# Kernel tuning notes

Hardware: AMD Instinct MI355X
Metric: run time of the kernel (lower is better)

The kernel has to match this reference:

```python
import jax, jax.numpy as jnp
import numpy as np

EPS = 1.55e-5  # tf.math.l2_normalize epsilon semantics: x / sqrt(max(sum(x^2), eps))


def _l2norm_tokens(t):
    # normalize over the token axis (-2), matching tf.math.l2_normalize(axis=-2)
    sq = jnp.sum(t * t, axis=-2, keepdims=True)
    return t * jax.lax.rsqrt(jnp.maximum(sq, EPS))


def setup_inputs() -> dict:
    key = jax.random.key(0)
    ks = jax.random.split(key, 4)
    B, H, W, C = 16, 64, 64, 512
    heads = 8
    return {
        "x": jax.random.normal(ks[0], (B, H, W, C), jnp.float32),
        "qkv_w": jax.random.normal(ks[1], (C, 3 * C), jnp.float32) * (C ** -0.5),
        "q_bias": jnp.zeros((C,), jnp.float32),
        "v_bias": jnp.zeros((C,), jnp.float32),
        "scale": jnp.ones((heads, 1, 1), jnp.float32),
        "proj_w": jax.random.normal(ks[2], (C, C), jnp.float32) * (C ** -0.5),
        "proj_b": jnp.zeros((C,), jnp.float32),
    }


def reference(x, qkv_w, q_bias, v_bias, scale, proj_w, proj_b):
    B, H, W, C = x.shape
    heads = scale.shape[0]
    d = C // heads
    N = H * W

    # 1x1 conv QKV (no conv bias) + concatenated [q_bias, 0, v_bias]
    qkv = jnp.einsum("bhwc,cf->bhwf", x, qkv_w)
    qkv = qkv + jnp.concatenate([q_bias, jnp.zeros_like(q_bias), v_bias])
    # [B, N, heads, 3, d] -> [B, heads, N, 3, d]
    qkv = qkv.reshape(B, N, heads, 3, d).transpose(0, 2, 1, 3, 4)
    q, k, v = qkv[..., 0, :], qkv[..., 1, :], qkv[..., 2, :]  # each [B, heads, N, d]

    q = _l2norm_tokens(q)
    k = _l2norm_tokens(k)

    # channel-attention: [B, heads, d, d]
    attn = jnp.einsum("bhnd,bhne->bhde", q * jnp.exp(scale), k)
    attn = jax.nn.softmax(attn, axis=-1)

    # matmul(attn, v^T) -> [B, heads, d, N]; perm [0,3,1,2] -> [B, N, heads, d]
    out = jnp.einsum("bhde,bhne->bhdn", attn, v)
    out = out.transpose(0, 3, 1, 2).reshape(B, H, W, C)

    # output 1x1 conv projection with bias
    return jnp.einsum("bhwc,cf->bhwf", out, proj_w) + proj_b
```

## Files before the change

### kernel.cpp

```cpp
#include <hip/hip_runtime.h>
#include <stdint.h>
#include <stddef.h>

#define BATCH  16
#define HEADS  8
#define NTOK   4096
#define CDIM   512
#define FDIM   1536

typedef short bf16x8 __attribute__((ext_vector_type(8)));
typedef float fx4    __attribute__((ext_vector_type(4)));

__device__ __forceinline__ uint16_t f2bf(float f) {
    uint32_t u = __float_as_uint(f);
    return (uint16_t)((u + 0x7FFFu + ((u >> 16) & 1u)) >> 16);
}
__device__ __forceinline__ float bf2f(uint16_t u) {
    return __uint_as_float(((uint32_t)u) << 16);
}
__device__ __forceinline__ void gload16(const uint16_t* g, uint16_t* l) {
    __builtin_amdgcn_global_load_lds(
        (const __attribute__((address_space(1))) uint32_t*)(g),
        (__attribute__((address_space(3))) uint32_t*)(l), 16, 0, 0);
}
__device__ __forceinline__ int cidx(int row, int col) {
    return row * 128 + (col ^ ((row & 7) << 3));
}

__global__ void transpose_w_kernel(const float* __restrict__ qkv_w,
                                   const float* __restrict__ proj_w,
                                   uint16_t* __restrict__ Wt,
                                   uint16_t* __restrict__ Pt) {
    __shared__ uint16_t tile[32][33];
    int blk = blockIdx.x;
    const float* src; uint16_t* dst; int W, Hh, r0, c0;
    if (blk < 768) {
        int tr = blk / 48, tc = blk % 48;
        src = qkv_w; dst = Wt; W = 1536; Hh = 512; r0 = tr * 32; c0 = tc * 32;
    } else {
        blk -= 768;
        int tr = blk / 16, tc = blk % 16;
        src = proj_w; dst = Pt; W = 512; Hh = 512; r0 = tr * 32; c0 = tc * 32;
    }
    const int tx = threadIdx.x & 31, ty = threadIdx.x >> 5;
    #pragma unroll
    for (int j = 0; j < 4; j++)
        tile[ty + 8 * j][tx] = f2bf(src[(size_t)(r0 + ty + 8 * j) * W + c0 + tx]);
    __syncthreads();
    #pragma unroll
    for (int j = 0; j < 4; j++)
        dst[(size_t)(c0 + ty + 8 * j) * Hh + r0 + tx] = tile[tx][ty + 8 * j];
}

__global__ void prep_kernel(const float* __restrict__ X,
                            uint16_t* __restrict__ Xb,
                            float* __restrict__ Sqk) {
    const int tid = blockIdx.x * blockDim.x + threadIdx.x;
    const int stride = gridDim.x * blockDim.x;
    for (int i = tid; i < (1 << 22); i += stride) {
        const fx4* src = reinterpret_cast<const fx4*>(X + (size_t)i * 8);
        fx4 v0 = src[0], v1 = src[1];
        union { bf16x8 v; uint16_t u[8]; } pk;
        #pragma unroll
        for (int e = 0; e < 4; e++) { pk.u[e] = f2bf(v0[e]); pk.u[4 + e] = f2bf(v1[e]); }
        reinterpret_cast<bf16x8*>(Xb)[i] = pk.v;
    }
    for (int i = tid; i < 16384; i += stride) Sqk[i] = 0.0f;
}

__global__ __launch_bounds__(256) void gemm_qkv_kernel(
        const uint16_t* __restrict__ Xb, const uint16_t* __restrict__ Wt,
        const float* __restrict__ q_bias, const float* __restrict__ v_bias,
        uint16_t* __restrict__ QT, uint16_t* __restrict__ KT,
        uint16_t* __restrict__ VT,
        float* __restrict__ Sq, float* __restrict__ Sk) {
    __shared__ uint16_t sh[128 * 128];
    uint16_t* As = sh;
    uint16_t* Bs = sh + 8192;
    const int bx = blockIdx.x;
    const int swz = (bx & 7) * 768 + (bx >> 3);
    const int tm = swz / 12, tn = swz % 12;
    const int gm = tm * 128, gn = tn * 128;
    const int b = gm >> 12, tok0 = gm & 4095;
    const int t = threadIdx.x, lane = t & 63, w = t >> 6;
    const int wm = w >> 1, wn = w & 1;
    const int l15 = lane & 15, lg = lane >> 4;
    fx4 acc[4][4] = {};
    const int skey = (t >> 3) & 7;
    const int scol0 = ((t & 7) ^ skey) * 8;
    for (int k0 = 0; k0 < 512; k0 += 64) {
        const uint16_t* ga = Xb + (size_t)(gm + (t >> 3)) * 512 + k0 + scol0;
        const uint16_t* gb = Wt + (size_t)(gn + (t >> 3)) * 512 + k0 + scol0;
        uint16_t* la = &As[t * 8];
        uint16_t* lb = &Bs[t * 8];
        #pragma unroll
        for (int j = 0; j < 4; j++) {
            gload16(ga + (size_t)j * 32 * 512, la + j * 2048);
            gload16(gb + (size_t)j * 32 * 512, lb + j * 2048);
        }
        __syncthreads();
        #pragma unroll
        for (int ks = 0; ks < 2; ks++) {
            const int kof = ks * 32 + lg * 8;
            bf16x8 af[4], bfr[4];
            #pragma unroll
            for (int m = 0; m < 4; m++) {
                const int row = wm * 64 + m * 16 + l15;
                af[m] = *reinterpret_cast<const bf16x8*>(&As[row * 64 + (kof ^ ((row & 7) << 3))]);
            }
            #pragma unroll
            for (int n = 0; n < 4; n++) {
                const int row = wn * 64 + n * 16 + l15;
                bfr[n] = *reinterpret_cast<const bf16x8*>(&Bs[row * 64 + (kof ^ ((row & 7) << 3))]);
            }
            #pragma unroll
            for (int m = 0; m < 4; m++)
                #pragma unroll
                for (int n = 0; n < 4; n++)
                    acc[m][n] = __builtin_amdgcn_mfma_f32_16x16x32_bf16(
                        af[m], bfr[n], acc[m][n], 0, 0, 0);
        }
        __syncthreads();
    }
    #pragma unroll
    for (int n = 0; n < 4; n++) {
        const int col = gn + wn * 64 + n * 16 + l15;
        const float bias = (col < 512) ? q_bias[col]
                          : ((col < 1024) ? 0.0f : v_bias[col - 1024]);
        #pragma unroll
        for (int m = 0; m < 4; m++)
            #pragma unroll
            for (int r = 0; r < 4; r++) {
                const int lrow = wm * 64 + m * 16 + lg * 4 + r;
                const int lcol = wn * 64 + n * 16 + l15;
                sh[cidx(lrow, lcol)] = f2bf(acc[m][n][r] + bias);
            }
    }
    __syncthreads();
    const int cc = t >> 7, tloc = t & 127;
    const int u = (gn >> 6) + cc;
    const int h = u / 3, which = u % 3;
    const int bh = b * 8 + h;
    if (which < 2) {
        const int d = tloc & 63, oct = tloc >> 6;
        uint16_t* dst = (which == 0 ? QT : KT)
                        + ((size_t)bh * 64 + d) * 4096 + tok0 + oct * 64;
        float ss = 0.f;
        #pragma unroll
        for (int g = 0; g < 8; g++) {
            union { bf16x8 v; uint16_t u16v[8]; } pk;
            #pragma unroll
            for (int s2 = 0; s2 < 8; s2++) {
                uint16_t val = sh[cidx(oct * 64 + g * 8 + s2, cc * 64 + d)];
                pk.u16v[s2] = val;
                float f = bf2f(val);
                ss += f * f;
            }
            *reinterpret_cast<bf16x8*>(dst + g * 8) = pk.v;
        }
        atomicAdd((which == 0 ? Sq : Sk) + bh * 64 + d, ss);
    } else {
        const int tok = tloc;
        uint16_t* dst = VT + (size_t)(gm + tok) * 512 + h * 64;
        #pragma unroll
        for (int bb = 0; bb < 8; bb++) {
            bf16x8 v = *reinterpret_cast<const bf16x8*>(&sh[cidx(tok, cc * 64 + bb * 8)]);
            *reinterpret_cast<bf16x8*>(dst + bb * 8) = v;
        }
    }
}

__global__ __launch_bounds__(256) void attn_qk_kernel(
        const uint16_t* __restrict__ QT, const uint16_t* __restrict__ KT,
        float* __restrict__ Gpart) {
    __shared__ uint16_t Qs[64 * 128];
    __shared__ uint16_t Ks[64 * 128];
    const int blk = blockIdx.x;
    const int bh = blk >> 2, quarter = blk & 3;
    const int t = threadIdx.x, lane = t & 63, w = t >> 6;
    const int l15 = lane & 15, lg = lane >> 4;
    const int wr = w >> 1, wc = w & 1;
    fx4 acc[2][2] = {};
    const uint16_t* qbase = QT + (size_t)bh * 64 * 4096;
    const uint16_t* kbase = KT + (size_t)bh * 64 * 4096;
    for (int it = 0; it < 8; it++) {
        const int tokt = quarter * 1024 + it * 128;
        #pragma unroll
        for (int j = 0; j < 4; j++) {
            const int li = j * 256 + t;
            const int row = li >> 4;
            const int src_off = (((li & 15) ^ (row & 7)) << 3);
            gload16(qbase + (size_t)row * 4096 + tokt + src_off, &Qs[li * 8]);
            gload16(kbase + (size_t)row * 4096 + tokt + src_off, &Ks[li * 8]);
        }
        __syncthreads();
        #pragma unroll
        for (int ks = 0; ks < 4; ks++) {
            const int kof = ks * 32 + lg * 8;
            const int ra0 = wr * 32 + l15,      ra1 = wr * 32 + 16 + l15;
            const int rb0 = wc * 32 + l15,      rb1 = wc * 32 + 16 + l15;
            bf16x8 a0 = *reinterpret_cast<const bf16x8*>(&Qs[ra0 * 128 + (kof ^ ((ra0 & 7) << 3))]);
            bf16x8 a1 = *reinterpret_cast<const bf16x8*>(&Qs[ra1 * 128 + (kof ^ ((ra1 & 7) << 3))]);
            bf16x8 b0 = *reinterpret_cast<const bf16x8*>(&Ks[rb0 * 128 + (kof ^ ((rb0 & 7) << 3))]);
            bf16x8 b1 = *reinterpret_cast<const bf16x8*>(&Ks[rb1 * 128 + (kof ^ ((rb1 & 7) << 3))]);
            acc[0][0] = __builtin_amdgcn_mfma_f32_16x16x32_bf16(a0, b0, acc[0][0], 0, 0, 0);
            acc[0][1] = __builtin_amdgcn_mfma_f32_16x16x32_bf16(a0, b1, acc[0][1], 0, 0, 0);
            acc[1][0] = __builtin_amdgcn_mfma_f32_16x16x32_bf16(a1, b0, acc[1][0], 0, 0, 0);
            acc[1][1] = __builtin_amdgcn_mfma_f32_16x16x32_bf16(a1, b1, acc[1][1], 0, 0, 0);
        }
        __syncthreads();
    }
    float* gp = Gpart + (size_t)quarter * 524288 + (size_t)bh * 4096;
    #pragma unroll
    for (int mi = 0; mi < 2; mi++)
        #pragma unroll
        for (int ni = 0; ni < 2; ni++)
            #pragma unroll
            for (int r = 0; r < 4; r++) {
                const int d = wr * 32 + mi * 16 + lg * 4 + r;
                const int e = wc * 32 + ni * 16 + l15;
                gp[d * 64 + e] = acc[mi][ni][r];
            }
}

__global__ void attn_finalize_kernel(const float* __restrict__ Gpart,
                                     const float* __restrict__ Sq,
                                     const float* __restrict__ Sk,
                                     const float* __restrict__ scale,
                                     uint16_t* __restrict__ attnb) {
    const int bh = blockIdx.x;
    const int h = bh & 7;
    const int t = threadIdx.x;
    const int e = t & 63, w = t >> 6;
    const float es = expf(scale[h]);
    const float rk = rsqrtf(fmaxf(Sk[bh * 64 + e], 1.55e-5f));
    const float* g0 = Gpart + (size_t)bh * 4096;
    for (int d = w; d < 64; d += 4) {
        const float rq = rsqrtf(fmaxf(Sq[bh * 64 + d], 1.55e-5f));
        float g = g0[d * 64 + e] + g0[524288 + d * 64 + e]
                + g0[1048576 + d * 64 + e] + g0[1572864 + d * 64 + e];
        float x = es * g * rq * rk;
        float m = x;
        #pragma unroll
        for (int off = 32; off; off >>= 1) m = fmaxf(m, __shfl_xor(m, off, 64));
        float p = expf(x - m);
        float s = p;
        #pragma unroll
        for (int off = 32; off; off >>= 1) s += __shfl_xor(s, off, 64);
        attnb[(size_t)bh * 4096 + d * 64 + e] = f2bf(p / s);
    }
}

__global__ __launch_bounds__(256) void pv_kernel(
        const uint16_t* __restrict__ VT, const uint16_t* __restrict__ attnb,
        uint16_t* __restrict__ out_t) {
    __shared__ uint16_t Vs[64 * 64];
    const int blk = blockIdx.x;
    const int bh = blk >> 6, chunk = blk & 63;
    const int b = bh >> 3, h = bh & 7;
    const int n0 = chunk * 64;
    const int t = threadIdx.x, lane = t & 63, w = t >> 6;
    const int l15 = lane & 15, lg = lane >> 4;
    #pragma unroll
    for (int j = 0; j < 2; j++) {
        const int li = j * 256 + t;
        const int row = li >> 3;
        const int src_off = (((li & 7) ^ (row & 7)) << 3);
        gload16(VT + (size_t)(b * NTOK + n0 + row) * 512 + h * 64 + src_off, &Vs[li * 8]);
    }
    bf16x8 bfr[4][2];
    const uint16_t* ab = attnb + (size_t)bh * 4096;
    #pragma unroll
    for (int n = 0; n < 4; n++)
        #pragma unroll
        for (int ks = 0; ks < 2; ks++)
            bfr[n][ks] = *reinterpret_cast<const bf16x8*>(ab + (n * 16 + l15) * 64 + ks * 32 + lg * 8);
    __syncthreads();
    fx4 acc[4] = {};
    #pragma unroll
    for (int ks = 0; ks < 2; ks++) {
        const int row = w * 16 + l15;
        const int kof = ks * 32 + lg * 8;
        bf16x8 a = *reinterpret_cast<const bf16x8*>(&Vs[row * 64 + (kof ^ ((row & 7) << 3))]);
        #pragma unroll
        for (int n = 0; n < 4; n++)
            acc[n] = __builtin_amdgcn_mfma_f32_16x16x32_bf16(a, bfr[n][ks], acc[n], 0, 0, 0);
    }
    #pragma unroll
    for (int n = 0; n < 4; n++)
        #pragma unroll
        for (int r = 0; r < 4; r++) {
            const int tokg = b * NTOK + n0 + w * 16 + lg * 4 + r;
            out_t[(size_t)tokg * CDIM + h * 64 + n * 16 + l15] = f2bf(acc[n][r]);
        }
}

__global__ __launch_bounds__(256) void gemm_proj_kernel(
        const uint16_t* __restrict__ At, const uint16_t* __restrict__ Pt,
        const float* __restrict__ proj_b, float* __restrict__ outp) {
    __shared__ uint16_t As[128 * 64];
    __shared__ uint16_t Bs[128 * 64];
    const int bx = blockIdx.x;
    const int swz = (bx & 7) * 256 + (bx >> 3);
    const int tn = swz & 3, tm = swz >> 2;
    const int gm = tm * 128, gn = tn * 128;
    const int t = threadIdx.x, lane = t & 63, w = t >> 6;
    const int wm = w >> 1, wn = w & 1;
    const int l15 = lane & 15, lg = lane >> 4;
    fx4 acc[4][4] = {};
    const int skey = (t >> 3) & 7;
    const int scol0 = ((t & 7) ^ skey) * 8;
    for (int k0 = 0; k0 < 512; k0 += 64) {
        const uint16_t* ga = At + (size_t)(gm + (t >> 3)) * 512 + k0 + scol0;
        const uint16_t* gb = Pt + (size_t)(gn + (t >> 3)) * 512 + k0 + scol0;
        #pragma unroll
        for (int j = 0; j < 4; j++) {
            gload16(ga + (size_t)j * 32 * 512, &As[t * 8 + j * 2048]);
            gload16(gb + (size_t)j * 32 * 512, &Bs[t * 8 + j * 2048]);
        }
        __syncthreads();
        #pragma unroll
        for (int ks = 0; ks < 2; ks++) {
            const int kof = ks * 32 + lg * 8;
            bf16x8 af[4], bfr[4];
            #pragma unroll
            for (int m = 0; m < 4; m++) {
                const int row = wm * 64 + m * 16 + l15;
                af[m] = *reinterpret_cast<const bf16x8*>(&As[row * 64 + (kof ^ ((row & 7) << 3))]);
            }
            #pragma unroll
            for (int n = 0; n < 4; n++) {
                const int row = wn * 64 + n * 16 + l15;
                bfr[n] = *reinterpret_cast<const bf16x8*>(&Bs[row * 64 + (kof ^ ((row & 7) << 3))]);
            }
            #pragma unroll
            for (int m = 0; m < 4; m++)
                #pragma unroll
                for (int n = 0; n < 4; n++)
                    acc[m][n] = __builtin_amdgcn_mfma_f32_16x16x32_bf16(
                        af[m], bfr[n], acc[m][n], 0, 0, 0);
        }
        __syncthreads();
    }
    #pragma unroll
    for (int m = 0; m < 4; m++) {
        #pragma unroll
        for (int n = 0; n < 4; n++) {
            const int col = gn + wn * 64 + n * 16 + l15;
            const float bias = proj_b[col];
            #pragma unroll
            for (int r = 0; r < 4; r++) {
                const int row = gm + wm * 64 + m * 16 + lg * 4 + r;
                outp[(size_t)row * CDIM + col] = acc[m][n][r] + bias;
            }
        }
    }
}

extern "C" void kernel_launch(void* const* d_in, const int* in_sizes, int n_in,
                              void* d_out, int out_size, void* d_ws, size_t ws_size,
                              hipStream_t stream) {
    (void)in_sizes; (void)n_in; (void)out_size; (void)ws_size;
    const float* x      = (const float*)d_in[0];
    const float* qkv_w  = (const float*)d_in[1];
    const float* q_bias = (const float*)d_in[2];
    const float* v_bias = (const float*)d_in[3];
    const float* scale  = (const float*)d_in[4];
    const float* proj_w = (const float*)d_in[5];
    const float* proj_b = (const float*)d_in[6];
    float* out = (float*)d_out;

    char* wsp = (char*)d_ws;
    uint16_t* Wt    = (uint16_t*)(wsp);
    uint16_t* Pt    = (uint16_t*)(wsp + 1572864);
    float*    Sq    = (float*)   (wsp + 2097152);
    float*    Sk    = (float*)   (wsp + 2129920);
    float*    Gpart = (float*)   (wsp + 2162688);
    uint16_t* attnb = (uint16_t*)(wsp + 10551296);
    uint16_t* QT    = (uint16_t*)(wsp + 11599872);
    uint16_t* KT    = (uint16_t*)(wsp + 78708736);
    uint16_t* VT    = (uint16_t*)(wsp + 145817600);
    uint16_t* Xb    = (uint16_t*)(wsp + 212926464);
    uint16_t* out_t = Xb;

    hipLaunchKernelGGL(transpose_w_kernel, dim3(1024), dim3(256), 0, stream,
                       qkv_w, proj_w, Wt, Pt);
    hipLaunchKernelGGL(prep_kernel, dim3(2048), dim3(256), 0, stream,
                       x, Xb, Sq);
    hipLaunchKernelGGL(gemm_qkv_kernel, dim3(6144), dim3(256), 0, stream,
                       Xb, Wt, q_bias, v_bias, QT, KT, VT, Sq, Sk);
    hipLaunchKernelGGL(attn_qk_kernel, dim3(512), dim3(256), 0, stream,
                       QT, KT, Gpart);
    hipLaunchKernelGGL(attn_finalize_kernel, dim3(128), dim3(256), 0, stream,
                       Gpart, Sq, Sk, scale, attnb);
    hipLaunchKernelGGL(pv_kernel, dim3(8192), dim3(256), 0, stream,
                       VT, attnb, out_t);
    hipLaunchKernelGGL(gemm_proj_kernel, dim3(2048), dim3(256), 0, stream,
                       out_t, Pt, proj_b, out);
}
```

Before: 578.5 us.

## Pipeline QKV and projection GEMMs with 4-stage LDS ring, stage PV output through LDS

After: 545.5 us. 1.06x faster.

```diff
diff --git a/kernel.cpp b/kernel.cpp
--- a/kernel.cpp
+++ b/kernel.cpp
@@ -74,9 +74,7 @@
         uint16_t* __restrict__ QT, uint16_t* __restrict__ KT,
         uint16_t* __restrict__ VT,
         float* __restrict__ Sq, float* __restrict__ Sk) {
-    __shared__ uint16_t sh[128 * 128];
-    uint16_t* As = sh;
-    uint16_t* Bs = sh + 8192;
+    __shared__ uint16_t ring[4][8192];
     const int bx = blockIdx.x;
     const int swz = (bx & 7) * 768 + (bx >> 3);
     const int tm = swz / 12, tn = swz % 12;
@@ -86,42 +84,50 @@
     const int wm = w >> 1, wn = w & 1;
     const int l15 = lane & 15, lg = lane >> 4;
     fx4 acc[4][4] = {};
-    const int skey = (t >> 3) & 7;
-    const int scol0 = ((t & 7) ^ skey) * 8;
-    for (int k0 = 0; k0 < 512; k0 += 64) {
-        const uint16_t* ga = Xb + (size_t)(gm + (t >> 3)) * 512 + k0 + scol0;
-        const uint16_t* gb = Wt + (size_t)(gn + (t >> 3)) * 512 + k0 + scol0;
-        uint16_t* la = &As[t * 8];
-        uint16_t* lb = &Bs[t * 8];
-        #pragma unroll
-        for (int j = 0; j < 4; j++) {
-            gload16(ga + (size_t)j * 32 * 512, la + j * 2048);
-            gload16(gb + (size_t)j * 32 * 512, lb + j * 2048);
-        }
-        __syncthreads();
-        #pragma unroll
-        for (int ks = 0; ks < 2; ks++) {
-            const int kof = ks * 32 + lg * 8;
-            bf16x8 af[4], bfr[4];
-            #pragma unroll
-            for (int m = 0; m < 4; m++) {
-                const int row = wm * 64 + m * 16 + l15;
-                af[m] = *reinterpret_cast<const bf16x8*>(&As[row * 64 + (kof ^ ((row & 7) << 3))]);
-            }
-            #pragma unroll
-            for (int n = 0; n < 4; n++) {
-                const int row = wn * 64 + n * 16 + l15;
-                bfr[n] = *reinterpret_cast<const bf16x8*>(&Bs[row * 64 + (kof ^ ((row & 7) << 3))]);
-            }
-            #pragma unroll
-            for (int m = 0; m < 4; m++)
-                #pragma unroll
-                for (int n = 0; n < 4; n++)
-                    acc[m][n] = __builtin_amdgcn_mfma_f32_16x16x32_bf16(
-                        af[m], bfr[n], acc[m][n], 0, 0, 0);
-        }
-        __syncthreads();
-    }
+    const int srow = t >> 2;
+    const int scol = (((t & 3) ^ (srow & 3)) << 3);
+    const uint16_t* gA = Xb + (size_t)(gm + srow) * 512 + scol;
+    const uint16_t* gB = Wt + (size_t)(gn + srow) * 512 + scol;
+#define STAGE_QKV(kt_) do {                                                   \
+        const int s_ = (kt_) & 3; const int k0_ = (kt_) * 32;                 \
+        gload16(gA + k0_,                 &ring[s_][t * 8]);                  \
+        gload16(gA + (size_t)64*512 + k0_, &ring[s_][t * 8 + 2048]);          \
+        gload16(gB + k0_,                 &ring[s_][4096 + t * 8]);           \
+        gload16(gB + (size_t)64*512 + k0_, &ring[s_][4096 + t * 8 + 2048]);   \
+    } while (0)
+    STAGE_QKV(0); STAGE_QKV(1); STAGE_QKV(2);
+    #pragma unroll
+    for (int kt = 0; kt < 16; ++kt) {
+        if (kt < 14)       asm volatile("s_waitcnt vmcnt(8) lgkmcnt(0)" ::: "memory");
+        else if (kt == 14) asm volatile("s_waitcnt vmcnt(4) lgkmcnt(0)" ::: "memory");
+        else               asm volatile("s_waitcnt vmcnt(0) lgkmcnt(0)" ::: "memory");
+        __builtin_amdgcn_s_barrier();
+        if (kt < 13) STAGE_QKV(kt + 3);
+        const uint16_t* As = &ring[kt & 3][0];
+        const uint16_t* Bs = &ring[kt & 3][4096];
+        bf16x8 af[4], bfr[4];
+        #pragma unroll
+        for (int m = 0; m < 4; m++) {
+            const int row = wm * 64 + m * 16 + l15;
+            af[m] = *reinterpret_cast<const bf16x8*>(&As[row * 32 + ((lg ^ (row & 3)) << 3)]);
+        }
+        #pragma unroll
+        for (int n = 0; n < 4; n++) {
+            const int row = wn * 64 + n * 16 + l15;
+            bfr[n] = *reinterpret_cast<const bf16x8*>(&Bs[row * 32 + ((lg ^ (row & 3)) << 3)]);
+        }
+        __builtin_amdgcn_s_setprio(1);
+        #pragma unroll
+        for (int m = 0; m < 4; m++)
+            #pragma unroll
+            for (int n = 0; n < 4; n++)
+                acc[m][n] = __builtin_amdgcn_mfma_f32_16x16x32_bf16(
+                    af[m], bfr[n], acc[m][n], 0, 0, 0);
+        __builtin_amdgcn_s_setprio(0);
+    }
+#undef STAGE_QKV
+    __syncthreads();
+    uint16_t* sh = &ring[0][0];
     #pragma unroll
     for (int n = 0; n < 4; n++) {
         const int col = gn + wn * 64 + n * 16 + l15;
@@ -255,6 +261,7 @@
         const uint16_t* __restrict__ VT, const uint16_t* __restrict__ attnb,
         uint16_t* __restrict__ out_t) {
     __shared__ uint16_t Vs[64 * 64];
+    __shared__ uint16_t Os[64 * 64];
     const int blk = blockIdx.x;
     const int bh = blk >> 6, chunk = blk & 63;
     const int b = bh >> 3, h = bh & 7;
@@ -290,16 +297,28 @@
     for (int n = 0; n < 4; n++)
         #pragma unroll
         for (int r = 0; r < 4; r++) {
-            const int tokg = b * NTOK + n0 + w * 16 + lg * 4 + r;
-            out_t[(size_t)tokg * CDIM + h * 64 + n * 16 + l15] = f2bf(acc[n][r]);
-        }
+            const int row = w * 16 + lg * 4 + r;
+            const int col = n * 16 + l15;
+            Os[row * 64 + (col ^ ((row & 7) << 3))] = f2bf(acc[n][r]);
+        }
+    __syncthreads();
+    {
+        const int tr = t >> 2, c0 = (t & 3) * 16;
+        uint16_t* orow = out_t + (size_t)(b * NTOK + n0 + tr) * CDIM + h * 64;
+        #pragma unroll
+        for (int cc2 = 0; cc2 < 2; cc2++) {
+            const int c = c0 + cc2 * 8;
+            const int chnk = (c >> 3) ^ (tr & 7);
+            bf16x8 vv = *reinterpret_cast<const bf16x8*>(&Os[tr * 64 + (chnk << 3)]);
+            *reinterpret_cast<bf16x8*>(orow + c) = vv;
+        }
+    }
 }
 
 __global__ __launch_bounds__(256) void gemm_proj_kernel(
         const uint16_t* __restrict__ At, const uint16_t* __restrict__ Pt,
         const float* __restrict__ proj_b, float* __restrict__ outp) {
-    __shared__ uint16_t As[128 * 64];
-    __shared__ uint16_t Bs[128 * 64];
+    __shared__ uint16_t ring[4][8192];
     const int bx = blockIdx.x;
     const int swz = (bx & 7) * 256 + (bx >> 3);
     const int tn = swz & 3, tm = swz >> 2;
@@ -308,40 +327,48 @@
     const int wm = w >> 1, wn = w & 1;
     const int l15 = lane & 15, lg = lane >> 4;
     fx4 acc[4][4] = {};
-    const int skey = (t >> 3) & 7;
-    const int scol0 = ((t & 7) ^ skey) * 8;
-    for (int k0 = 0; k0 < 512; k0 += 64) {
-        const uint16_t* ga = At + (size_t)(gm + (t >> 3)) * 512 + k0 + scol0;
-        const uint16_t* gb = Pt + (size_t)(gn + (t >> 3)) * 512 + k0 + scol0;
-        #pragma unroll
-        for (int j = 0; j < 4; j++) {
-            gload16(ga + (size_t)j * 32 * 512, &As[t * 8 + j * 2048]);
-            gload16(gb + (size_t)j * 32 * 512, &Bs[t * 8 + j * 2048]);
-        }
-        __syncthreads();
-        #pragma unroll
-        for (int ks = 0; ks < 2; ks++) {
-            const int kof = ks * 32 + lg * 8;
-            bf16x8 af[4], bfr[4];
-            #pragma unroll
-            for (int m = 0; m < 4; m++) {
-                const int row = wm * 64 + m * 16 + l15;
-                af[m] = *reinterpret_cast<const bf16x8*>(&As[row * 64 + (kof ^ ((row & 7) << 3))]);
-            }
-            #pragma unroll
-            for (int n = 0; n < 4; n++) {
-                const int row = wn * 64 + n * 16 + l15;
-                bfr[n] = *reinterpret_cast<const bf16x8*>(&Bs[row * 64 + (kof ^ ((row & 7) << 3))]);
-            }
-            #pragma unroll
-            for (int m = 0; m < 4; m++)
-                #pragma unroll
-                for (int n = 0; n < 4; n++)
-                    acc[m][n] = __builtin_amdgcn_mfma_f32_16x16x32_bf16(
-                        af[m], bfr[n], acc[m][n], 0, 0, 0);
-        }
-        __syncthreads();
-    }
+    const int srow = t >> 2;
+    const int scol = (((t & 3) ^ (srow & 3)) << 3);
+    const uint16_t* gA = At + (size_t)(gm + srow) * 512 + scol;
+    const uint16_t* gB = Pt + (size_t)(gn + srow) * 512 + scol;
+#define STAGE_PROJ(kt_) do {                                                  \
+        const int s_ = (kt_) & 3; const int k0_ = (kt_) * 32;                 \
+        gload16(gA + k0_,                 &ring[s_][t * 8]);                  \
+        gload16(gA + (size_t)64*512 + k0_, &ring[s_][t * 8 + 2048]);          \
+        gload16(gB + k0_,                 &ring[s_][4096 + t * 8]);           \
+        gload16(gB + (size_t)64*512 + k0_, &ring[s_][4096 + t * 8 + 2048]);   \
+    } while (0)
+    STAGE_PROJ(0); STAGE_PROJ(1); STAGE_PROJ(2);
+    #pragma unroll
+    for (int kt = 0; kt < 16; ++kt) {
+        if (kt < 14)       asm volatile("s_waitcnt vmcnt(8) lgkmcnt(0)" ::: "memory");
+        else if (kt == 14) asm volatile("s_waitcnt vmcnt(4) lgkmcnt(0)" ::: "memory");
+        else               asm volatile("s_waitcnt vmcnt(0) lgkmcnt(0)" ::: "memory");
+        __builtin_amdgcn_s_barrier();
+        if (kt < 13) STAGE_PROJ(kt + 3);
+        const uint16_t* As = &ring[kt & 3][0];
+        const uint16_t* Bs = &ring[kt & 3][4096];
+        bf16x8 af[4], bfr[4];
+        #pragma unroll
+        for (int m = 0; m < 4; m++) {
+            const int row = wm * 64 + m * 16 + l15;
+            af[m] = *reinterpret_cast<const bf16x8*>(&As[row * 32 + ((lg ^ (row & 3)) << 3)]);
+        }
+        #pragma unroll
+        for (int n = 0; n < 4; n++) {
+            const int row = wn * 64 + n * 16 + l15;
+            bfr[n] = *reinterpret_cast<const bf16x8*>(&Bs[row * 32 + ((lg ^ (row & 3)) << 3)]);
+        }
+        __builtin_amdgcn_s_setprio(1);
+        #pragma unroll
+        for (int m = 0; m < 4; m++)
+            #pragma unroll
+            for (int n = 0; n < 4; n++)
+                acc[m][n] = __builtin_amdgcn_mfma_f32_16x16x32_bf16(
+                    af[m], bfr[n], acc[m][n], 0, 0, 0);
+        __builtin_amdgcn_s_setprio(0);
+    }
+#undef STAGE_PROJ
     #pragma unroll
     for (int m = 0; m < 4; m++) {
         #pragma unroll
```
